# Kernel optimization log

Measured on AMD Instinct MI355X. Metric: run time of the kernel, lower is better.

## Reference

```python
import jax, jax.numpy as jnp
import numpy as np

B, T, C, H = 2, 2048, 1024, 16
D = C // H  # head dim = 64


def setup_inputs() -> dict:
    key = jax.random.key(0)
    k1, k2, k3 = jax.random.split(key, 3)
    s = 1.0 / np.sqrt(C)
    return {
        "x": jax.random.normal(k1, (B, T, C), dtype=jnp.float32),
        "w_qkv": jax.random.normal(k2, (C, 3 * C), dtype=jnp.float32) * s,
        "b_qkv": jnp.zeros((3 * C,), dtype=jnp.float32),
        "w_proj": jax.random.normal(k3, (C, C), dtype=jnp.float32) * s,
        "b_proj": jnp.zeros((C,), dtype=jnp.float32),
    }


def reference(x, w_qkv, b_qkv, w_proj, b_proj):
    Bx, Tx, Cx = x.shape
    qkv = x @ w_qkv + b_qkv                      # [B,T,3C]
    q, k, v = jnp.split(qkv, 3, axis=-1)         # each [B,T,C]
    # split heads -> [B,H,T,D]
    q = q.reshape(Bx, Tx, H, D).transpose(0, 2, 1, 3)
    k = k.reshape(Bx, Tx, H, D).transpose(0, 2, 1, 3)
    v = v.reshape(Bx, Tx, H, D).transpose(0, 2, 1, 3)
    att = jnp.einsum("bhqd,bhkd->bhqk", q, k) * (1.0 / np.sqrt(D))
    causal = jnp.tril(jnp.ones((Tx, Tx), dtype=bool))
    att = jnp.where(causal, att, -jnp.inf)
    att = jax.nn.softmax(att, axis=-1)
    y = jnp.einsum("bhqk,bhkd->bhqd", att, v)    # [B,H,T,D]
    y = y.transpose(0, 2, 1, 3).reshape(Bx, Tx, Cx)
    return y @ w_proj + b_proj
```

## Files before the change

kernel.cpp:

```cpp
#include <hip/hip_runtime.h>


typedef __attribute__((ext_vector_type(8))) __bf16 bf16x8;
typedef __attribute__((ext_vector_type(4))) float f32x4;
typedef __attribute__((ext_vector_type(8))) unsigned short u16x8;
typedef __attribute__((ext_vector_type(4))) unsigned short u16x4;

#define GAS __attribute__((address_space(1)))
#define LAS __attribute__((address_space(3)))

__device__ __forceinline__ unsigned short f2b(float f) {
  unsigned int u = __float_as_uint(f);
  unsigned int r = 0x7FFFu + ((u >> 16) & 1u);
  return (unsigned short)((u + r) >> 16);
}
__device__ __forceinline__ float b2f(unsigned short u) {
  return __uint_as_float((unsigned int)u << 16);
}


__global__ void cvt_f32_to_bf16(const float* __restrict__ src,
                                unsigned short* __restrict__ dst, int n4) {
  int i = blockIdx.x * blockDim.x + threadIdx.x;
  if (i < n4) {
    float4 v = ((const float4*)src)[i];
    u16x4 o = { f2b(v.x), f2b(v.y), f2b(v.z), f2b(v.w) };
    *(u16x4*)(dst + (size_t)i * 4) = o;
  }
}

__global__ void transpose_f32_to_bf16(const float* __restrict__ src,
                                      unsigned short* __restrict__ dst,
                                      int K, int N) {
  __shared__ float tile[32][33];
  int n0 = blockIdx.x * 32, k0 = blockIdx.y * 32;
  int tx = threadIdx.x, ty = threadIdx.y;
#pragma unroll
  for (int i = 0; i < 32; i += 8)
    tile[ty + i][tx] = src[(size_t)(k0 + ty + i) * N + n0 + tx];
  __syncthreads();
#pragma unroll
  for (int i = 0; i < 32; i += 8)
    dst[(size_t)(n0 + ty + i) * K + k0 + tx] = f2b(tile[tx][ty + i]);
}


template <int MODE>
__global__ void __launch_bounds__(256) gemm_bt(
    const unsigned short* __restrict__ A, const unsigned short* __restrict__ Bt,
    const float* __restrict__ bias,
    unsigned short* __restrict__ Oq, unsigned short* __restrict__ Ok,
    unsigned short* __restrict__ Ov, float* __restrict__ Of,
    int M, int N, int K) {
  __shared__ unsigned short smem[4 * 128 * 64];
  unsigned short* As = smem;
  unsigned short* Bs = smem + 2 * 128 * 64;

  const int tid = threadIdx.x;
  const int lane = tid & 63;
  const int wid = tid >> 6;
  const int wr = wid >> 1, wc = wid & 1;
  const int lr = lane & 15, lg = lane >> 4;
  const int m0 = blockIdx.x * 128;
  const int n0 = blockIdx.y * 128;

  f32x4 acc[4][4];
#pragma unroll
  for (int mi = 0; mi < 4; mi++)
#pragma unroll
    for (int ni = 0; ni < 4; ni++) acc[mi][ni] = (f32x4){0.f, 0.f, 0.f, 0.f};

  auto stage = [&](int t, int buf) {
    const int k0 = t * 64;
    unsigned short* Ad = As + buf * (128 * 64);
    unsigned short* Bd = Bs + buf * (128 * 64);
#pragma unroll
    for (int it = 0; it < 4; ++it) {
      const int chunk_u = it * 256 + (tid & ~63);
      const int chunk = chunk_u + lane;
      const int row = chunk >> 3;
      const int col = ((chunk & 7) ^ (row & 7)) * 8;
      __builtin_amdgcn_global_load_lds(
          (GAS unsigned int*)(A + (size_t)(m0 + row) * K + k0 + col),
          (LAS unsigned int*)(Ad + chunk_u * 8), 16, 0, 0);
      __builtin_amdgcn_global_load_lds(
          (GAS unsigned int*)(Bt + (size_t)(n0 + row) * K + k0 + col),
          (LAS unsigned int*)(Bd + chunk_u * 8), 16, 0, 0);
    }
  };

  const int swa = (lr & 7) * 8;
  const int kt = K >> 6;

  stage(0, 0);

  for (int t = 0; t < kt; ++t) {
    const int cur = t & 1;
    __builtin_amdgcn_s_barrier();
    if (t + 1 < kt) {
      stage(t + 1, cur ^ 1);
      asm volatile("s_waitcnt vmcnt(8)" ::: "memory");
    } else {
      asm volatile("s_waitcnt vmcnt(0)" ::: "memory");
    }
    __builtin_amdgcn_s_barrier();

    const unsigned short* Ab = As + cur * (128 * 64);
    const unsigned short* Bb = Bs + cur * (128 * 64);

#pragma unroll
    for (int kk = 0; kk < 2; ++kk) {
      bf16x8 af[4], bfr[4];
#pragma unroll
      for (int mi = 0; mi < 4; mi++)
        af[mi] = *(const bf16x8*)(Ab + (wr * 64 + mi * 16 + lr) * 64 +
                                  ((kk * 32 + lg * 8) ^ swa));
#pragma unroll
      for (int ni = 0; ni < 4; ni++)
        bfr[ni] = *(const bf16x8*)(Bb + (wc * 64 + ni * 16 + lr) * 64 +
                                   ((kk * 32 + lg * 8) ^ swa));
      __builtin_amdgcn_s_setprio(1);
#pragma unroll
      for (int mi = 0; mi < 4; mi++)
#pragma unroll
        for (int ni = 0; ni < 4; ni++)
          acc[mi][ni] = __builtin_amdgcn_mfma_f32_16x16x32_bf16(
              af[mi], bfr[ni], acc[mi][ni], 0, 0, 0);
      __builtin_amdgcn_s_setprio(0);
    }
  }

  const float SCLQ = 0.125f * 1.44269504088896340736f;

  if constexpr (MODE == 1) {
#pragma unroll
    for (int mi = 0; mi < 4; mi++) {
#pragma unroll
      for (int ni = 0; ni < 4; ni++) {
        const int nn = n0 + wc * 64 + ni * 16 + lr;
        const float bv = bias[nn];
#pragma unroll
        for (int r = 0; r < 4; r++) {
          const int mm = m0 + wr * 64 + mi * 16 + lg * 4 + r;
          Of[(size_t)mm * N + nn] = acc[mi][ni][r] + bv;
        }
      }
    }
  } else {
    unsigned short* L = smem;
    const int which = n0 >> 10;
    const float sc = (which == 0) ? SCLQ : 1.0f;
    __syncthreads();
#pragma unroll
    for (int mi = 0; mi < 4; mi++) {
#pragma unroll
      for (int ni = 0; ni < 4; ni++) {
        const int nn_l = wc * 64 + ni * 16 + lr;
        const float bv = bias[n0 + nn_l];
#pragma unroll
        for (int r = 0; r < 4; r++) {
          const int mm_l = wr * 64 + mi * 16 + lg * 4 + r;
          const unsigned short v = f2b((acc[mi][ni][r] + bv) * sc);
          if (which == 2) L[nn_l * 136 + mm_l] = v;
          else            L[mm_l * 136 + nn_l] = v;
        }
      }
    }
    __syncthreads();
    const int b = m0 >> 11;
    const int t0 = m0 & 2047;
    const int h0 = (n0 & 1023) >> 6;
    if (which == 2) {
      const int row = tid >> 1;
      const int hsub = row >> 6, d = row & 63;
      const int tt0 = (tid & 1) * 64;
      const unsigned short* src = L + row * 136 + tt0;
      unsigned short* dst = Ov +
          ((size_t)((b * 16 + h0 + hsub) * 64 + d)) * 2048 + t0 + tt0;
#pragma unroll
      for (int j = 0; j < 8; j++)
        *(u16x8*)(dst + j * 8) = *(const u16x8*)(src + j * 8);
    } else {
      const int mm_l = tid & 127;
      const int hsub = tid >> 7;
      const unsigned short* src = L + mm_l * 136 + hsub * 64;
      unsigned short* base = (which == 0) ? Oq : Ok;
      unsigned short* dst = base +
          ((size_t)(b * 16 + h0 + hsub) * 2048 + t0 + mm_l) * 64;
#pragma unroll
      for (int j = 0; j < 8; j++)
        *(u16x8*)(dst + j * 8) = *(const u16x8*)(src + j * 8);
    }
  }
}


__global__ void __launch_bounds__(512) attn_kernel(
    const unsigned short* __restrict__ Qh, const unsigned short* __restrict__ Kh,
    const unsigned short* __restrict__ Vh, unsigned short* __restrict__ yatt,
    unsigned short* __restrict__ Opart, float* __restrict__ Mp,
    float* __restrict__ Lp) {
  __shared__ unsigned short KsL[2 * 64 * 64];
  __shared__ unsigned short VsL[2 * 64 * 64];
  __shared__ unsigned short Pl[8 * 16 * 72];

  const int tid = threadIdx.x;
  const int lane = tid & 63;
  const int w = tid >> 6;
  const int lr = lane & 15, lg = lane >> 4;

  const int cls = blockIdx.x >> 5;
  const int bh = blockIdx.x & 31;
  const int hh = bh & 15;
  const int bb = bh >> 4;

  const unsigned long long QA = 0x8899AABBCCDDEEFFull;
  const unsigned long long QB = 0x0000014425566377ull;
  const unsigned long long KK = 0x00A4912444444444ull;
  const int qt = (cls < 16) ? (int)((QA >> (4 * cls)) & 15)
                            : (int)((QB >> (4 * (cls - 16))) & 15);
  const int kind = (int)((KK >> (2 * cls)) & 3);
  const int t0 = (kind == 1) ? (qt + 1) : 0;
  const int t1 = (kind == 0) ? (qt + 1) : (2 * qt + 2);

  const size_t head_base = ((size_t)(bb * 16 + hh)) * 2048 * 64;
  const unsigned short* Qg = Qh + head_base;
  const unsigned short* Kg = Kh + head_base;
  const unsigned short* Vg = Vh + head_base;

  const int q0 = qt * 128 + w * 16;
  const int diagw = 2 * qt + ((w >> 2) & 1);

  bf16x8 aq0 = *(const bf16x8*)(Qg + (size_t)(q0 + lr) * 64 + lg * 8);
  bf16x8 aq1 = *(const bf16x8*)(Qg + (size_t)(q0 + lr) * 64 + 32 + lg * 8);

  bf16x8 vones;
#pragma unroll
  for (int j = 0; j < 8; j++) vones[j] = (__bf16)1.0f;

  float m_run[4], l_run[4];
  f32x4 acc_o[4];
#pragma unroll
  for (int r = 0; r < 4; r++) { m_run[r] = -__builtin_inff(); l_run[r] = 0.f; }
#pragma unroll
  for (int dj = 0; dj < 4; dj++) acc_o[dj] = (f32x4){0.f, 0.f, 0.f, 0.f};

  const int srow = tid >> 3;
  const int scol = (((tid & 7) ^ (srow & 7)) << 3);

  auto stage = [&](int kv0, int buf) {
    unsigned short* Kd = KsL + buf * (64 * 64);
    unsigned short* Vd = VsL + buf * (64 * 64);
    const int base_u = (tid & ~63) * 8;
    __builtin_amdgcn_global_load_lds(
        (GAS unsigned int*)(Kg + (size_t)(kv0 + srow) * 64 + scol),
        (LAS unsigned int*)(Kd + base_u), 16, 0, 0);
    __builtin_amdgcn_global_load_lds(
        (GAS unsigned int*)(Vg + (size_t)srow * 2048 + kv0 + scol),
        (LAS unsigned int*)(Vd + base_u), 16, 0, 0);
  };

  __bf16* Pw = (__bf16*)(Pl + w * 16 * 72);
  const int swr = (lr & 7) << 3;

  stage(t0 * 64, t0 & 1);

  for (int i = t0; i < t1; ++i) {
    const int cur = i & 1;
    __builtin_amdgcn_s_barrier();
    if (i + 1 < t1) {
      stage((i + 1) * 64, cur ^ 1);
      asm volatile("s_waitcnt vmcnt(2)" ::: "memory");
    } else {
      asm volatile("s_waitcnt vmcnt(0)" ::: "memory");
    }
    __builtin_amdgcn_s_barrier();

    if (i <= diagw) {
      const int kv0 = i * 64;
      const unsigned short* Kb = KsL + cur * (64 * 64);
      const unsigned short* Vb = VsL + cur * (64 * 64);

      f32x4 s[4];
      __builtin_amdgcn_s_setprio(1);
#pragma unroll
      for (int nj = 0; nj < 4; nj++) {
        const unsigned short* krow = Kb + (nj * 16 + lr) * 64;
        bf16x8 kb0 = *(const bf16x8*)(krow + ((lg * 8) ^ swr));
        bf16x8 kb1 = *(const bf16x8*)(krow + ((32 + lg * 8) ^ swr));
        f32x4 z = (f32x4){0.f, 0.f, 0.f, 0.f};
        z = __builtin_amdgcn_mfma_f32_16x16x32_bf16(aq0, kb0, z, 0, 0, 0);
        z = __builtin_amdgcn_mfma_f32_16x16x32_bf16(aq1, kb1, z, 0, 0, 0);
        s[nj] = z;
      }
      __builtin_amdgcn_s_setprio(0);

      if (i == diagw) {
#pragma unroll
        for (int nj = 0; nj < 4; nj++) {
          const int key = kv0 + nj * 16 + lr;
#pragma unroll
          for (int r = 0; r < 4; r++) {
            const int qrow = q0 + lg * 4 + r;
            if (key > qrow) s[nj][r] = -__builtin_inff();
          }
        }
      }

      float pm[4];
#pragma unroll
      for (int r = 0; r < 4; r++)
        pm[r] = fmaxf(fmaxf(s[0][r], s[1][r]), fmaxf(s[2][r], s[3][r]));

      const bool okl = (pm[0] <= m_run[0] + 8.f) & (pm[1] <= m_run[1] + 8.f) &
                       (pm[2] <= m_run[2] + 8.f) & (pm[3] <= m_run[3] + 8.f);
      if (!__all(okl)) {
#pragma unroll
        for (int r = 0; r < 4; r++) {
#pragma unroll
          for (int off = 1; off < 16; off <<= 1)
            pm[r] = fmaxf(pm[r], __shfl_xor(pm[r], off));
          const float mn = fmaxf(m_run[r], pm[r]);
          const float sc = exp2f(m_run[r] - mn);
          m_run[r] = mn;
          l_run[r] *= sc;
#pragma unroll
          for (int dj = 0; dj < 4; dj++) acc_o[dj][r] *= sc;
        }
      }

#pragma unroll
      for (int nj = 0; nj < 4; nj++) {
#pragma unroll
        for (int r = 0; r < 4; r++) {
          const float p = exp2f(s[nj][r] - m_run[r]);
          Pw[(lg * 4 + r) * 72 + nj * 16 + lr] = (__bf16)p;
        }
      }

      bf16x8 pa0 = *(const bf16x8*)(Pw + lr * 72 + lg * 8);
      bf16x8 pa1 = *(const bf16x8*)(Pw + lr * 72 + 32 + lg * 8);

      __builtin_amdgcn_s_setprio(1);
      f32x4 zs = (f32x4){0.f, 0.f, 0.f, 0.f};
      zs = __builtin_amdgcn_mfma_f32_16x16x32_bf16(pa0, vones, zs, 0, 0, 0);
      zs = __builtin_amdgcn_mfma_f32_16x16x32_bf16(pa1, vones, zs, 0, 0, 0);

#pragma unroll
      for (int dj = 0; dj < 4; dj++) {
        const unsigned short* vrow = Vb + (dj * 16 + lr) * 64;
        bf16x8 vb0 = *(const bf16x8*)(vrow + ((lg * 8) ^ swr));
        bf16x8 vb1 = *(const bf16x8*)(vrow + ((32 + lg * 8) ^ swr));
        acc_o[dj] = __builtin_amdgcn_mfma_f32_16x16x32_bf16(pa0, vb0, acc_o[dj], 0, 0, 0);
        acc_o[dj] = __builtin_amdgcn_mfma_f32_16x16x32_bf16(pa1, vb1, acc_o[dj], 0, 0, 0);
      }
      __builtin_amdgcn_s_setprio(0);

#pragma unroll
      for (int r = 0; r < 4; r++) l_run[r] += zs[r];
    }
  }

  if (kind == 2) {
    __bf16* yb = (__bf16*)yatt;
#pragma unroll
    for (int r = 0; r < 4; r++) {
      const float inv = 1.0f / l_run[r];
      const int t = q0 + lg * 4 + r;
      const size_t rowbase = ((size_t)(bb * 2048 + t)) * 1024 + hh * 64;
#pragma unroll
      for (int dj = 0; dj < 4; dj++)
        yb[rowbase + dj * 16 + lr] = (__bf16)(acc_o[dj][r] * inv);
    }
  } else {
    __bf16* Ob = (__bf16*)Opart;
#pragma unroll
    for (int r = 0; r < 4; r++) {
      const int slot = bh * 1536 + (q0 + lg * 4 + r) - 512;
      const size_t obase = ((size_t)(kind * 49152 + slot)) * 64;
#pragma unroll
      for (int dj = 0; dj < 4; dj++)
        Ob[obase + dj * 16 + lr] = (__bf16)acc_o[dj][r];
      if (lr == 0) {
        Mp[kind * 49152 + slot] = m_run[r];
        Lp[kind * 49152 + slot] = l_run[r];
      }
    }
  }
}

__global__ void __launch_bounds__(256) attn_merge(
    const unsigned short* __restrict__ Op, const float* __restrict__ Mp,
    const float* __restrict__ Lp, unsigned short* __restrict__ yatt) {
  const int gid = blockIdx.x * 256 + threadIdx.x;
  const int sl = gid >> 3;
  const int d0 = (gid & 7) * 8;
  const int bh = blockIdx.y;
  const int slot = bh * 1536 + sl;
  const float m1 = Mp[slot], m2 = Mp[49152 + slot];
  const float l1 = Lp[slot], l2 = Lp[49152 + slot];
  const float mx = fmaxf(m1, m2);
  const float w1 = exp2f(m1 - mx), w2 = exp2f(m2 - mx);
  const float inv = 1.0f / (l1 * w1 + l2 * w2);
  u16x8 a = *(const u16x8*)(Op + (size_t)slot * 64 + d0);
  u16x8 b = *(const u16x8*)(Op + (size_t)(49152 + slot) * 64 + d0);
  const int qr = 512 + sl;
  unsigned short* dst = yatt +
      ((size_t)((bh >> 4) * 2048 + qr)) * 1024 + (bh & 15) * 64 + d0;
  u16x8 o;
#pragma unroll
  for (int j = 0; j < 8; j++)
    o[j] = f2b((b2f(a[j]) * w1 + b2f(b[j]) * w2) * inv);
  *(u16x8*)dst = o;
}


extern "C" void kernel_launch(void* const* d_in, const int* in_sizes, int n_in,
                              void* d_out, int out_size, void* d_ws,
                              size_t ws_size, hipStream_t stream) {
  (void)in_sizes; (void)n_in; (void)out_size; (void)ws_size;
  const float* x      = (const float*)d_in[0];
  const float* w_qkv  = (const float*)d_in[1];
  const float* b_qkv  = (const float*)d_in[2];
  const float* w_proj = (const float*)d_in[3];
  const float* b_proj = (const float*)d_in[4];
  float* out = (float*)d_out;

  unsigned short* ws     = (unsigned short*)d_ws;
  unsigned short* xb     = ws;
  unsigned short* wqkvT  = xb     + (size_t)4096 * 1024;
  unsigned short* wprojT = wqkvT  + (size_t)3072 * 1024;
  unsigned short* Qh     = wprojT + (size_t)1024 * 1024;
  unsigned short* Kh     = Qh     + (size_t)2 * 16 * 2048 * 64;
  unsigned short* Vh     = Kh     + (size_t)2 * 16 * 2048 * 64;
  unsigned short* yatt   = Vh     + (size_t)2 * 16 * 2048 * 64;

  unsigned short* Opart = ws;
  float* Mp = (float*)(ws + (size_t)6291456);
  float* Lp = Mp + 2 * 49152;

  cvt_f32_to_bf16<<<4096, 256, 0, stream>>>(x, xb, 1048576);
  transpose_f32_to_bf16<<<dim3(96, 32), dim3(32, 8), 0, stream>>>(w_qkv, wqkvT, 1024, 3072);
  transpose_f32_to_bf16<<<dim3(32, 32), dim3(32, 8), 0, stream>>>(w_proj, wprojT, 1024, 1024);

  gemm_bt<0><<<dim3(32, 24), 256, 0, stream>>>(xb, wqkvT, b_qkv, Qh, Kh, Vh,
                                               nullptr, 4096, 3072, 1024);
  attn_kernel<<<896, 512, 0, stream>>>(Qh, Kh, Vh, yatt, Opart, Mp, Lp);
  attn_merge<<<dim3(48, 32), 256, 0, stream>>>(Opart, Mp, Lp, yatt);
  gemm_bt<1><<<dim3(32, 8), 256, 0, stream>>>(yatt, wprojT, b_proj, nullptr,
                                              nullptr, nullptr, out, 4096, 1024, 1024);
}
```

Before: 121.2 us.

## Give each attention wave two query tiles with transposed S layout

The attention kernel drops from 8 waves to 4 waves per block, and each wave now processes 32 query rows as two 16-row tiles. Every K and V fragment read from LDS therefore feeds twice as many MFMAs. QK^T is computed transposed (K as the A operand), so each lane holds one query row's scores: the row max needs only two cross-lane shuffles, and the row sum is accumulated directly instead of through a ones-vector MFMA. The trade-off is more registers per wave and fewer waves per block to hide latency, which launch_bounds(256,3) and the now two-iteration staging loop try to offset.

Result: faster. 117.9 us (-2.7%).

```diff
diff --git a/kernel.cpp b/kernel.cpp
--- a/kernel.cpp
+++ b/kernel.cpp
@@ -2,6 +2,7 @@
 
 
 typedef __attribute__((ext_vector_type(8))) __bf16 bf16x8;
+typedef __attribute__((ext_vector_type(4))) __bf16 bf16x4;
 typedef __attribute__((ext_vector_type(4))) float f32x4;
 typedef __attribute__((ext_vector_type(8))) unsigned short u16x8;
 typedef __attribute__((ext_vector_type(4))) unsigned short u16x4;
@@ -195,14 +196,14 @@
 }
 
 
-__global__ void __launch_bounds__(512) attn_kernel(
+__global__ void __launch_bounds__(256, 3) attn_kernel(
     const unsigned short* __restrict__ Qh, const unsigned short* __restrict__ Kh,
     const unsigned short* __restrict__ Vh, unsigned short* __restrict__ yatt,
     unsigned short* __restrict__ Opart, float* __restrict__ Mp,
     float* __restrict__ Lp) {
   __shared__ unsigned short KsL[2 * 64 * 64];
   __shared__ unsigned short VsL[2 * 64 * 64];
-  __shared__ unsigned short Pl[8 * 16 * 72];
+  __shared__ unsigned short Pl[4 * 32 * 72];
 
   const int tid = threadIdx.x;
   const int lane = tid & 63;
@@ -228,39 +229,42 @@
   const unsigned short* Kg = Kh + head_base;
   const unsigned short* Vg = Vh + head_base;
 
-  const int q0 = qt * 128 + w * 16;
-  const int diagw = 2 * qt + ((w >> 2) & 1);
-
-  bf16x8 aq0 = *(const bf16x8*)(Qg + (size_t)(q0 + lr) * 64 + lg * 8);
-  bf16x8 aq1 = *(const bf16x8*)(Qg + (size_t)(q0 + lr) * 64 + 32 + lg * 8);
-
-  bf16x8 vones;
-#pragma unroll
-  for (int j = 0; j < 8; j++) vones[j] = (__bf16)1.0f;
-
-  float m_run[4], l_run[4];
-  f32x4 acc_o[4];
-#pragma unroll
-  for (int r = 0; r < 4; r++) { m_run[r] = -__builtin_inff(); l_run[r] = 0.f; }
-#pragma unroll
-  for (int dj = 0; dj < 4; dj++) acc_o[dj] = (f32x4){0.f, 0.f, 0.f, 0.f};
-
-  const int srow = tid >> 3;
-  const int scol = (((tid & 7) ^ (srow & 7)) << 3);
+  const int q0 = qt * 128 + w * 32;
+  const int diagw = 2 * qt + (w >> 1);
+
+  bf16x8 aqA0 = *(const bf16x8*)(Qg + (size_t)(q0 + lr) * 64 + lg * 8);
+  bf16x8 aqA1 = *(const bf16x8*)(Qg + (size_t)(q0 + lr) * 64 + 32 + lg * 8);
+  bf16x8 aqB0 = *(const bf16x8*)(Qg + (size_t)(q0 + 16 + lr) * 64 + lg * 8);
+  bf16x8 aqB1 = *(const bf16x8*)(Qg + (size_t)(q0 + 16 + lr) * 64 + 32 + lg * 8);
+
+  float mA = -__builtin_inff(), mB = -__builtin_inff();
+  float lA = 0.f, lB = 0.f;
+  f32x4 oA[4], oB[4];
+#pragma unroll
+  for (int dj = 0; dj < 4; dj++) {
+    oA[dj] = (f32x4){0.f, 0.f, 0.f, 0.f};
+    oB[dj] = (f32x4){0.f, 0.f, 0.f, 0.f};
+  }
 
   auto stage = [&](int kv0, int buf) {
     unsigned short* Kd = KsL + buf * (64 * 64);
     unsigned short* Vd = VsL + buf * (64 * 64);
-    const int base_u = (tid & ~63) * 8;
-    __builtin_amdgcn_global_load_lds(
-        (GAS unsigned int*)(Kg + (size_t)(kv0 + srow) * 64 + scol),
-        (LAS unsigned int*)(Kd + base_u), 16, 0, 0);
-    __builtin_amdgcn_global_load_lds(
-        (GAS unsigned int*)(Vg + (size_t)srow * 2048 + kv0 + scol),
-        (LAS unsigned int*)(Vd + base_u), 16, 0, 0);
+#pragma unroll
+    for (int it = 0; it < 2; ++it) {
+      const int chunk_u = it * 256 + (tid & ~63);
+      const int chunk = chunk_u + lane;
+      const int row = chunk >> 3;
+      const int col = ((chunk & 7) ^ (row & 7)) << 3;
+      __builtin_amdgcn_global_load_lds(
+          (GAS unsigned int*)(Kg + (size_t)(kv0 + row) * 64 + col),
+          (LAS unsigned int*)(Kd + chunk_u * 8), 16, 0, 0);
+      __builtin_amdgcn_global_load_lds(
+          (GAS unsigned int*)(Vg + (size_t)row * 2048 + kv0 + col),
+          (LAS unsigned int*)(Vd + chunk_u * 8), 16, 0, 0);
+    }
   };
 
-  __bf16* Pw = (__bf16*)(Pl + w * 16 * 72);
+  __bf16* Pw = (__bf16*)(Pl + w * 32 * 72);
   const int swr = (lr & 7) << 3;
 
   stage(t0 * 64, t0 & 1);
@@ -270,7 +274,7 @@
     __builtin_amdgcn_s_barrier();
     if (i + 1 < t1) {
       stage((i + 1) * 64, cur ^ 1);
-      asm volatile("s_waitcnt vmcnt(2)" ::: "memory");
+      asm volatile("s_waitcnt vmcnt(4)" ::: "memory");
     } else {
       asm volatile("s_waitcnt vmcnt(0)" ::: "memory");
     }
@@ -281,110 +285,141 @@
       const unsigned short* Kb = KsL + cur * (64 * 64);
       const unsigned short* Vb = VsL + cur * (64 * 64);
 
-      f32x4 s[4];
+      f32x4 sA[4], sB[4];
       __builtin_amdgcn_s_setprio(1);
 #pragma unroll
       for (int nj = 0; nj < 4; nj++) {
         const unsigned short* krow = Kb + (nj * 16 + lr) * 64;
         bf16x8 kb0 = *(const bf16x8*)(krow + ((lg * 8) ^ swr));
         bf16x8 kb1 = *(const bf16x8*)(krow + ((32 + lg * 8) ^ swr));
-        f32x4 z = (f32x4){0.f, 0.f, 0.f, 0.f};
-        z = __builtin_amdgcn_mfma_f32_16x16x32_bf16(aq0, kb0, z, 0, 0, 0);
-        z = __builtin_amdgcn_mfma_f32_16x16x32_bf16(aq1, kb1, z, 0, 0, 0);
-        s[nj] = z;
+        f32x4 zA = (f32x4){0.f, 0.f, 0.f, 0.f};
+        f32x4 zB = (f32x4){0.f, 0.f, 0.f, 0.f};
+        zA = __builtin_amdgcn_mfma_f32_16x16x32_bf16(kb0, aqA0, zA, 0, 0, 0);
+        zA = __builtin_amdgcn_mfma_f32_16x16x32_bf16(kb1, aqA1, zA, 0, 0, 0);
+        zB = __builtin_amdgcn_mfma_f32_16x16x32_bf16(kb0, aqB0, zB, 0, 0, 0);
+        zB = __builtin_amdgcn_mfma_f32_16x16x32_bf16(kb1, aqB1, zB, 0, 0, 0);
+        sA[nj] = zA;
+        sB[nj] = zB;
       }
       __builtin_amdgcn_s_setprio(0);
 
       if (i == diagw) {
+        const int qrA = q0 + lr, qrB = q0 + 16 + lr;
 #pragma unroll
         for (int nj = 0; nj < 4; nj++) {
-          const int key = kv0 + nj * 16 + lr;
 #pragma unroll
           for (int r = 0; r < 4; r++) {
-            const int qrow = q0 + lg * 4 + r;
-            if (key > qrow) s[nj][r] = -__builtin_inff();
+            const int key = kv0 + nj * 16 + lg * 4 + r;
+            if (key > qrA) sA[nj][r] = -__builtin_inff();
+            if (key > qrB) sB[nj][r] = -__builtin_inff();
           }
         }
       }
 
-      float pm[4];
-#pragma unroll
-      for (int r = 0; r < 4; r++)
-        pm[r] = fmaxf(fmaxf(s[0][r], s[1][r]), fmaxf(s[2][r], s[3][r]));
-
-      const bool okl = (pm[0] <= m_run[0] + 8.f) & (pm[1] <= m_run[1] + 8.f) &
-                       (pm[2] <= m_run[2] + 8.f) & (pm[3] <= m_run[3] + 8.f);
+      float pmA = sA[0][0], pmB = sB[0][0];
+#pragma unroll
+      for (int nj = 0; nj < 4; nj++)
+#pragma unroll
+        for (int r = 0; r < 4; r++) {
+          pmA = fmaxf(pmA, sA[nj][r]);
+          pmB = fmaxf(pmB, sB[nj][r]);
+        }
+
+      const bool okl = (pmA <= mA + 8.f) & (pmB <= mB + 8.f);
       if (!__all(okl)) {
+        pmA = fmaxf(pmA, __shfl_xor(pmA, 16));
+        pmA = fmaxf(pmA, __shfl_xor(pmA, 32));
+        pmB = fmaxf(pmB, __shfl_xor(pmB, 16));
+        pmB = fmaxf(pmB, __shfl_xor(pmB, 32));
+        const float mnA = fmaxf(mA, pmA), mnB = fmaxf(mB, pmB);
+        const float scA = exp2f(mA - mnA), scB = exp2f(mB - mnB);
+        mA = mnA; mB = mnB;
+        lA *= scA; lB *= scB;
 #pragma unroll
         for (int r = 0; r < 4; r++) {
-#pragma unroll
-          for (int off = 1; off < 16; off <<= 1)
-            pm[r] = fmaxf(pm[r], __shfl_xor(pm[r], off));
-          const float mn = fmaxf(m_run[r], pm[r]);
-          const float sc = exp2f(m_run[r] - mn);
-          m_run[r] = mn;
-          l_run[r] *= sc;
-#pragma unroll
-          for (int dj = 0; dj < 4; dj++) acc_o[dj][r] *= sc;
+          const float cA = __shfl(scA, lg * 4 + r);
+          const float cB = __shfl(scB, lg * 4 + r);
+#pragma unroll
+          for (int dj = 0; dj < 4; dj++) {
+            oA[dj][r] *= cA;
+            oB[dj][r] *= cB;
+          }
         }
       }
 
 #pragma unroll
       for (int nj = 0; nj < 4; nj++) {
-#pragma unroll
-        for (int r = 0; r < 4; r++) {
-          const float p = exp2f(s[nj][r] - m_run[r]);
-          Pw[(lg * 4 + r) * 72 + nj * 16 + lr] = (__bf16)p;
-        }
-      }
-
-      bf16x8 pa0 = *(const bf16x8*)(Pw + lr * 72 + lg * 8);
-      bf16x8 pa1 = *(const bf16x8*)(Pw + lr * 72 + 32 + lg * 8);
+        const float a0 = exp2f(sA[nj][0] - mA), a1 = exp2f(sA[nj][1] - mA);
+        const float a2 = exp2f(sA[nj][2] - mA), a3 = exp2f(sA[nj][3] - mA);
+        lA += (a0 + a1) + (a2 + a3);
+        bf16x4 pkA = {(__bf16)a0, (__bf16)a1, (__bf16)a2, (__bf16)a3};
+        *(bf16x4*)(Pw + lr * 72 + nj * 16 + lg * 4) = pkA;
+        const float b0 = exp2f(sB[nj][0] - mB), b1 = exp2f(sB[nj][1] - mB);
+        const float b2 = exp2f(sB[nj][2] - mB), b3 = exp2f(sB[nj][3] - mB);
+        lB += (b0 + b1) + (b2 + b3);
+        bf16x4 pkB = {(__bf16)b0, (__bf16)b1, (__bf16)b2, (__bf16)b3};
+        *(bf16x4*)(Pw + (16 + lr) * 72 + nj * 16 + lg * 4) = pkB;
+      }
+
+      bf16x8 paA0 = *(const bf16x8*)(Pw + lr * 72 + lg * 8);
+      bf16x8 paA1 = *(const bf16x8*)(Pw + lr * 72 + 32 + lg * 8);
+      bf16x8 paB0 = *(const bf16x8*)(Pw + (16 + lr) * 72 + lg * 8);
+      bf16x8 paB1 = *(const bf16x8*)(Pw + (16 + lr) * 72 + 32 + lg * 8);
 
       __builtin_amdgcn_s_setprio(1);
-      f32x4 zs = (f32x4){0.f, 0.f, 0.f, 0.f};
-      zs = __builtin_amdgcn_mfma_f32_16x16x32_bf16(pa0, vones, zs, 0, 0, 0);
-      zs = __builtin_amdgcn_mfma_f32_16x16x32_bf16(pa1, vones, zs, 0, 0, 0);
-
 #pragma unroll
       for (int dj = 0; dj < 4; dj++) {
         const unsigned short* vrow = Vb + (dj * 16 + lr) * 64;
         bf16x8 vb0 = *(const bf16x8*)(vrow + ((lg * 8) ^ swr));
         bf16x8 vb1 = *(const bf16x8*)(vrow + ((32 + lg * 8) ^ swr));
-        acc_o[dj] = __builtin_amdgcn_mfma_f32_16x16x32_bf16(pa0, vb0, acc_o[dj], 0, 0, 0);
-        acc_o[dj] = __builtin_amdgcn_mfma_f32_16x16x32_bf16(pa1, vb1, acc_o[dj], 0, 0, 0);
+        oA[dj] = __builtin_amdgcn_mfma_f32_16x16x32_bf16(paA0, vb0, oA[dj], 0, 0, 0);
+        oA[dj] = __builtin_amdgcn_mfma_f32_16x16x32_bf16(paA1, vb1, oA[dj], 0, 0, 0);
+        oB[dj] = __builtin_amdgcn_mfma_f32_16x16x32_bf16(paB0, vb0, oB[dj], 0, 0, 0);
+        oB[dj] = __builtin_amdgcn_mfma_f32_16x16x32_bf16(paB1, vb1, oB[dj], 0, 0, 0);
       }
       __builtin_amdgcn_s_setprio(0);
-
-#pragma unroll
-      for (int r = 0; r < 4; r++) l_run[r] += zs[r];
-    }
-  }
+    }
+  }
+
+  lA += __shfl_xor(lA, 16); lA += __shfl_xor(lA, 32);
+  lB += __shfl_xor(lB, 16); lB += __shfl_xor(lB, 32);
 
   if (kind == 2) {
     __bf16* yb = (__bf16*)yatt;
 #pragma unroll
     for (int r = 0; r < 4; r++) {
-      const float inv = 1.0f / l_run[r];
-      const int t = q0 + lg * 4 + r;
-      const size_t rowbase = ((size_t)(bb * 2048 + t)) * 1024 + hh * 64;
-#pragma unroll
-      for (int dj = 0; dj < 4; dj++)
-        yb[rowbase + dj * 16 + lr] = (__bf16)(acc_o[dj][r] * inv);
+      const float invA = 1.0f / __shfl(lA, lg * 4 + r);
+      const float invB = 1.0f / __shfl(lB, lg * 4 + r);
+      const int tA = q0 + lg * 4 + r;
+      const int tB = tA + 16;
+      const size_t baseA = ((size_t)(bb * 2048 + tA)) * 1024 + hh * 64;
+      const size_t baseB = ((size_t)(bb * 2048 + tB)) * 1024 + hh * 64;
+#pragma unroll
+      for (int dj = 0; dj < 4; dj++) {
+        yb[baseA + dj * 16 + lr] = (__bf16)(oA[dj][r] * invA);
+        yb[baseB + dj * 16 + lr] = (__bf16)(oB[dj][r] * invB);
+      }
     }
   } else {
     __bf16* Ob = (__bf16*)Opart;
 #pragma unroll
     for (int r = 0; r < 4; r++) {
-      const int slot = bh * 1536 + (q0 + lg * 4 + r) - 512;
-      const size_t obase = ((size_t)(kind * 49152 + slot)) * 64;
-#pragma unroll
-      for (int dj = 0; dj < 4; dj++)
-        Ob[obase + dj * 16 + lr] = (__bf16)acc_o[dj][r];
-      if (lr == 0) {
-        Mp[kind * 49152 + slot] = m_run[r];
-        Lp[kind * 49152 + slot] = l_run[r];
-      }
+      const int slotA = bh * 1536 + (q0 + lg * 4 + r) - 512;
+      const int slotB = slotA + 16;
+      const size_t baseA = ((size_t)(kind * 49152 + slotA)) * 64;
+      const size_t baseB = ((size_t)(kind * 49152 + slotB)) * 64;
+#pragma unroll
+      for (int dj = 0; dj < 4; dj++) {
+        Ob[baseA + dj * 16 + lr] = (__bf16)oA[dj][r];
+        Ob[baseB + dj * 16 + lr] = (__bf16)oB[dj][r];
+      }
+    }
+    if (lg == 0) {
+      const int slA = bh * 1536 + (q0 + lr) - 512;
+      Mp[kind * 49152 + slA] = mA;
+      Lp[kind * 49152 + slA] = lA;
+      Mp[kind * 49152 + slA + 16] = mB;
+      Lp[kind * 49152 + slA + 16] = lB;
     }
   }
 }
@@ -445,7 +480,7 @@
 
   gemm_bt<0><<<dim3(32, 24), 256, 0, stream>>>(xb, wqkvT, b_qkv, Qh, Kh, Vh,
                                                nullptr, 4096, 3072, 1024);
-  attn_kernel<<<896, 512, 0, stream>>>(Qh, Kh, Vh, yatt, Opart, Mp, Lp);
+  attn_kernel<<<896, 256, 0, stream>>>(Qh, Kh, Vh, yatt, Opart, Mp, Lp);
   attn_merge<<<dim3(48, 32), 256, 0, stream>>>(Opart, Mp, Lp, yatt);
   gemm_bt<1><<<dim3(32, 8), 256, 0, stream>>>(yatt, wprojT, b_proj, nullptr,
                                               nullptr, nullptr, out, 4096, 1024, 1024);
```
